# Kernel optimization log

Measured on AMD Instinct MI355X. Metric: run time of the kernel, lower is better.

## Reference

```python
import jax, jax.numpy as jnp
import numpy as np
from jax import lax

B, N, T, HOR, HID = 512, 128, 128, 32, 512


def _uni(k, shape, s):
    return jax.random.uniform(k, shape, jnp.float32, -s, s)


def setup_inputs() -> dict:
    key = jax.random.key(0)
    ks = jax.random.split(key, 24)
    s = 1.0 / np.sqrt(HID)
    inp = {"window": jax.random.normal(ks[0], (B * N, T), jnp.float32)}
    # encoder LSTM (2 layers, torch gate order i,f,g,o)
    inp["Wih0"] = _uni(ks[1], (4 * HID, N), s); inp["Whh0"] = _uni(ks[2], (4 * HID, HID), s)
    inp["bih0"] = _uni(ks[3], (4 * HID,), s);   inp["bhh0"] = _uni(ks[4], (4 * HID,), s)
    inp["Wih1"] = _uni(ks[5], (4 * HID, HID), s); inp["Whh1"] = _uni(ks[6], (4 * HID, HID), s)
    inp["bih1"] = _uni(ks[7], (4 * HID,), s);     inp["bhh1"] = _uni(ks[8], (4 * HID,), s)
    # decoder cells
    inp["Wc1i"] = _uni(ks[9], (4 * HID, N), s);   inp["Wc1h"] = _uni(ks[10], (4 * HID, HID), s)
    inp["bc1i"] = _uni(ks[11], (4 * HID,), s);    inp["bc1h"] = _uni(ks[12], (4 * HID,), s)
    inp["Wc2i"] = _uni(ks[13], (4 * HID, HID), s); inp["Wc2h"] = _uni(ks[14], (4 * HID, HID), s)
    inp["bc2i"] = _uni(ks[15], (4 * HID,), s);     inp["bc2h"] = _uni(ks[16], (4 * HID,), s)
    # output projection
    inp["Wp"] = _uni(ks[17], (N, HID), s); inp["bp"] = _uni(ks[18], (N,), s)
    # deterministic inverted-dropout masks
    keep_e = 0.75  # nn.LSTM inter-layer dropout p=0.25
    keep_d = 0.8   # F.dropout p=0.2 in decode loop
    inp["enc_mask"] = (jax.random.uniform(ks[19], (T, B, HID)) < keep_e).astype(jnp.float32) / keep_e
    inp["dec_h_mask"] = (jax.random.uniform(ks[20], (HOR - 1, B, HID)) < keep_d).astype(jnp.float32) / keep_d
    inp["dec_c_mask"] = (jax.random.uniform(ks[21], (HOR - 1, B, HID)) < keep_d).astype(jnp.float32) / keep_d
    return inp


def _cell(x, h, c, Wih, Whh, bih, bhh):
    g = x @ Wih.T + h @ Whh.T + (bih + bhh)
    i, f, gg, o = jnp.split(g, 4, axis=-1)
    c = jax.nn.sigmoid(f) * c + jax.nn.sigmoid(i) * jnp.tanh(gg)
    h = jax.nn.sigmoid(o) * jnp.tanh(c)
    return h, c


def _run_layer(xs, Wih, Whh, bih, bhh):
    # xs: [T, B, D] -> outputs [T, B, HID], final (h, c)
    h0 = jnp.zeros((xs.shape[1], HID), xs.dtype)
    def step(carry, x):
        h, c = carry
        h, c = _cell(x, h, c, Wih, Whh, bih, bhh)
        return (h, c), h
    (h, c), hs = lax.scan(step, (h0, h0), xs)
    return hs, h, c


def reference(window, Wih0, Whh0, bih0, bhh0, Wih1, Whh1, bih1, bhh1,
              Wc1i, Wc1h, bc1i, bc1h, Wc2i, Wc2h, bc2i, bc2h, Wp, bp,
              enc_mask, dec_h_mask, dec_c_mask):
    x = window.reshape(B, T, N).transpose(1, 0, 2)  # [T, B, N]
    hs0, h1, c1 = _run_layer(x, Wih0, Whh0, bih0, bhh0)
    hs0 = hs0 * enc_mask  # inter-layer dropout (training mode)
    _, h2, c2 = _run_layer(hs0, Wih1, Whh1, bih1, bhh1)

    def dec_step(carry, masks):
        h1, c1, h2, c2 = carry
        mh, mc = masks
        pred = h2 @ Wp.T + bp                       # [B, N]
        h1, c1 = _cell(pred, h1, c1, Wc1i, Wc1h, bc1i, bc1h)
        h1 = h1 * mh
        c1 = c1 * mc
        h2, c2 = _cell(h1, h2, c2, Wc2i, Wc2h, bc2i, bc2h)
        return (h1, c1, h2, c2), pred

    (h1, c1, h2, c2), preds = lax.scan(dec_step, (h1, c1, h2, c2), (dec_h_mask, dec_c_mask))
    final = h2 @ Wp.T + bp                          # [B, N]
    allp = jnp.concatenate([preds, final[None]], axis=0)  # [HOR, B, N]
    # torch: each pred.view(-1,1), cat dim=1 -> [B*N, HOR]
    return allp.transpose(1, 2, 0).reshape(B * N, HOR)
```

## Files before the change

kernel.cpp:

```cpp
#include <hip/hip_runtime.h>
#include <math.h>

#define HID 512
#define BAT 512
#define NIN 128
#define TST 128
#define HOR 32
#define SBZ ((size_t)BAT * HID)

using bf16x8 = __attribute__((ext_vector_type(8))) __bf16;
using f32x4  = __attribute__((ext_vector_type(4))) float;

__device__ __forceinline__ float sigf(float x) { return 1.0f / (1.0f + __expf(-x)); }
__device__ __forceinline__ float tanhfast(float x) { return 1.0f - 2.0f / (__expf(2.0f * x) + 1.0f); }

__device__ __forceinline__ short f2bf(float x) {
    union { float f; unsigned u; } v; v.f = x;
    unsigned r = (v.u + 0x7FFFu + ((v.u >> 16) & 1u)) >> 16;
    return (short)r;
}
__device__ __forceinline__ float bf2f(short s) {
    union { unsigned u; float f; } v; v.u = ((unsigned)(unsigned short)s) << 16;
    return v.f;
}
__device__ __forceinline__ bf16x8 asbf(f32x4 v) {
    union { f32x4 f; bf16x8 b; } u; u.f = v; return u.b;
}

__device__ __forceinline__ void gbar3(unsigned* bar, int bid, unsigned ep) {
    __syncthreads();
    if (threadIdx.x == 0) {
        unsigned* leaf = bar + ((unsigned)bid >> 3) * 32;
        unsigned* root = bar + 1024;
        unsigned* flag = bar + 1056;
        unsigned old = __hip_atomic_fetch_add(leaf, 1u, __ATOMIC_RELAXED, __HIP_MEMORY_SCOPE_AGENT);
        if (old == 8u * ep - 1u) {
            unsigned ro = __hip_atomic_fetch_add(root, 1u, __ATOMIC_RELAXED, __HIP_MEMORY_SCOPE_AGENT);
            if (ro == 32u * ep - 1u)
                __hip_atomic_store(flag, ep, __ATOMIC_RELAXED, __HIP_MEMORY_SCOPE_AGENT);
        }
        int spin = 0;
        while (__hip_atomic_load(flag, __ATOMIC_RELAXED, __HIP_MEMORY_SCOPE_AGENT) < ep) {
            __builtin_amdgcn_s_sleep(1);
            if (((++spin) & 63) == 0)
                __hip_atomic_fetch_add(flag, 0u, __ATOMIC_RELAXED, __HIP_MEMORY_SCOPE_AGENT);
        }
    }
    __syncthreads();
}


__global__ __launch_bounds__(256) void prep_w(const float* __restrict__ Wih,
                                              const float* __restrict__ Whh,
                                              short* __restrict__ W2, int Kx, int Kp) {
    size_t i = (size_t)blockIdx.x * 256 + threadIdx.x;
    if (i >= (size_t)2048 * Kp) return;
    int np = (int)(i / Kp), kp = (int)(i % Kp);
    int u = np >> 2, gate = np & 3;
    int on = gate * HID + u;
    float w = (kp < Kx) ? Wih[(size_t)on * Kx + kp] : Whh[(size_t)on * HID + (kp - Kx)];
    W2[i] = f2bf(w);
}

__global__ __launch_bounds__(256) void prep_x(const float* __restrict__ window,
                                              short* __restrict__ X2t) {
    size_t i = (size_t)blockIdx.x * 256 + threadIdx.x;
    if (i >= (size_t)TST * BAT * NIN) return;
    int n = (int)(i & 127);
    int b = (int)((i >> 7) & 511);
    int t = (int)(i >> 16);
    float x = window[(size_t)b * (TST * NIN) + (size_t)t * NIN + n];
    int rg = b >> 4;
    int l = (b & 15) + (((n >> 3) & 3) << 4);
    int e = n & 7;
    size_t base = (size_t)t * 65536 + ((size_t)(rg * 4 + (n >> 5)) << 9) + l * 8 + e;
    X2t[base] = f2bf(x);
}

__global__ __launch_bounds__(256) void prep_fuse(const float* __restrict__ Wc1i,
                                                 const float* __restrict__ Wp,
                                                 float* __restrict__ Wfuse) {
    size_t i = (size_t)blockIdx.x * 256 + threadIdx.x;
    if (i >= (size_t)2048 * 512) return;
    int on = (int)(i >> 9), k = (int)(i & 511);
    float s = 0.f;
    for (int n = 0; n < NIN; ++n) s += Wc1i[(size_t)on * NIN + n] * Wp[(size_t)n * HID + k];
    Wfuse[i] = s;
}

__global__ __launch_bounds__(256) void prep_badd(const float* __restrict__ Wc1i,
                                                 const float* __restrict__ bp,
                                                 float* __restrict__ badd) {
    int on = blockIdx.x * 256 + threadIdx.x;
    if (on >= 2048) return;
    float s = 0.f;
    for (int n = 0; n < NIN; ++n) s += Wc1i[(size_t)on * NIN + n] * bp[n];
    badd[on] = s;
}

__global__ __launch_bounds__(256) void prep_bias(const float* __restrict__ bih,
                                                 const float* __restrict__ bhh,
                                                 const float* __restrict__ badd,
                                                 float* __restrict__ bout) {
    int np = blockIdx.x * 256 + threadIdx.x;
    if (np >= 2048) return;
    int on = (np & 3) * HID + (np >> 2);
    float v = bih[on] + bhh[on];
    if (badd) v += badd[on];
    bout[np] = v;
}

__global__ __launch_bounds__(256) void prep_wp(const float* __restrict__ Wp,
                                               short* __restrict__ W2p) {
    int i = blockIdx.x * 256 + threadIdx.x;
    if (i >= 128 * 512) return;
    W2p[i] = f2bf(Wp[i]);
}


__device__ __forceinline__ void load_wres(char* lds, const short* Wg, int K) {
    const int tid = threadIdx.x;
    const int r = tid >> 4;
    const int cnt = K >> 7;
    const int jb = (tid & 15) * cnt;
    for (int q = 0; q < cnt; ++q) {
        int j = jb + q;
        bf16x8 v = *(const bf16x8*)(Wg + (size_t)r * K + j * 8);
        *(bf16x8*)(lds + j * 512 + r * 16) = v;
    }
}

__device__ __forceinline__ void pre_mask_asm(const float* msk, int mrow, int u0, float o[4]) {
    const int lane = threadIdx.x & 63;
    const float* p = msk + (size_t)(mrow + ((lane >> 3) << 2)) * HID + u0 + (lane & 7);
#pragma unroll
    for (int r = 0; r < 4; ++r)
        asm volatile("global_load_dword %0, %1, off" : "=v"(o[r]) : "v"(p + (size_t)r * HID));
}

template<int C0, int C1>
__device__ __forceinline__ void gemm_pipeC(
    const char* wres, const short* a0t, const short* a1t,
    int mb, f32x4 acc[2][2])
{
    constexpr int NKC = C0 + C1;
    constexpr int D = 16;
    const int lane = threadIdx.x & 63;
    const int arow = lane & 15, akg = lane >> 4;
    const size_t lb = (size_t)lane << 4;
    const char* base0 = (const char*)a0t;
    const char* base1 = (const char*)a1t;
    auto cptr = [&](int kc, int fh) -> const char* {
        return (kc < C0)
            ? base0 + (((size_t)(mb * 2 + fh) * C0 + kc) << 10) + lb
            : base1 + (((size_t)(mb * 2 + fh) * C1 + (kc - C0)) << 10) + lb;
    };
    f32x4 q0[D], q1[D];
#pragma unroll
    for (int i = 0; i < D; ++i) {
        asm volatile("global_load_dwordx4 %0, %1, off sc0 sc1" : "=v"(q0[i]) : "v"(cptr(i, 0)));
        asm volatile("global_load_dwordx4 %0, %1, off sc0 sc1" : "=v"(q1[i]) : "v"(cptr(i, 1)));
    }
#pragma unroll
    for (int kc = 0; kc < NKC; ++kc) {
        const int sl = kc % D;
        asm volatile("s_waitcnt vmcnt(%2)"
                     : "+v"(q0[sl]), "+v"(q1[sl])
                     : "i"((2 * ((NKC - kc) < D ? (NKC - kc) : D)) - 2));
        const bf16x8 fa0 = asbf(q0[sl]);
        const bf16x8 fa1 = asbf(q1[sl]);
        if (kc + D < NKC) {
            asm volatile("global_load_dwordx4 %0, %1, off sc0 sc1" : "=v"(q0[sl]) : "v"(cptr(kc + D, 0)));
            asm volatile("global_load_dwordx4 %0, %1, off sc0 sc1" : "=v"(q1[sl]) : "v"(cptr(kc + D, 1)));
        }
        const char* wrow = wres + (size_t)(((kc << 2) + akg) << 9);
        const bf16x8 fb0 = *(const bf16x8*)(wrow + (arow << 4));
        const bf16x8 fb1 = *(const bf16x8*)(wrow + ((16 + arow) << 4));
        acc[0][0] = __builtin_amdgcn_mfma_f32_16x16x32_bf16(fa0, fb0, acc[0][0], 0, 0, 0);
        acc[0][1] = __builtin_amdgcn_mfma_f32_16x16x32_bf16(fa0, fb1, acc[0][1], 0, 0, 0);
        acc[1][0] = __builtin_amdgcn_mfma_f32_16x16x32_bf16(fa1, fb0, acc[1][0], 0, 0, 0);
        acc[1][1] = __builtin_amdgcn_mfma_f32_16x16x32_bf16(fa1, fb1, acc[1][1], 0, 0, 0);
    }
    asm volatile("s_waitcnt vmcnt(0)");
}

__device__ __forceinline__ void cell_epi_r(
    char* scrw, f32x4 acc[2][2], float creg[4],
    int mb, int np0, const float* bias_p,
    const float* mh4, const float* mc4, const float* ma4,
    short* h2_out, short* h2_aux)
{
    const int lane = threadIdx.x & 63;
#pragma unroll
    for (int mi = 0; mi < 2; ++mi)
#pragma unroll
        for (int ni = 0; ni < 2; ++ni) {
            const int row = mi * 16 + ((lane >> 4) << 2);
            const int col = ni * 16 + (lane & 15);
#pragma unroll
            for (int r = 0; r < 4; ++r)
                *(float*)(scrw + (row + r) * 128 + (col << 2)) = acc[mi][ni][r];
        }
    asm volatile("s_waitcnt lgkmcnt(0)" ::: "memory");
    const int ul = lane & 7, g = lane >> 3;
    f32x4 gv[4];
#pragma unroll
    for (int r = 0; r < 4; ++r)
        gv[r] = *(const f32x4*)(scrw + ((g << 2) + r) * 128 + (ul << 4));
    asm volatile("s_waitcnt lgkmcnt(0)" ::: "memory");
    const float4 bs = *(const float4*)(bias_p + np0 + (ul << 2));
#pragma unroll
    for (int r = 0; r < 4; ++r) {
        const int m = (g << 2) + r;
        const int fh = m >> 4, r16 = m & 15;
        const float gi = gv[r][0] + bs.x, gf = gv[r][1] + bs.y;
        const float gg = gv[r][2] + bs.z, go = gv[r][3] + bs.w;
        const float cn = sigf(gf) * creg[r] + sigf(gi) * tanhfast(gg);
        const float h  = sigf(go) * tanhfast(cn);
        creg[r] = mc4 ? cn * mc4[r] : cn;
        const float hm = mh4 ? h * mh4[r] : h;
        const int idx2 = (r16 << 3) + ul;
        *(short*)(scrw + fh * 256 + idx2 * 2) = f2bf(hm);
        if (h2_aux)
            *(short*)(scrw + 512 + fh * 256 + idx2 * 2) = f2bf(h * ma4[r]);
    }
    const int u0l = np0 >> 2;
    const int c_hi = u0l >> 5, gsub = (u0l >> 3) & 3;
    unsigned vmain[2], vaux[2];
#pragma unroll
    for (int s = 0; s < 2; ++s)
        vmain[s] = *(const unsigned*)(scrw + s * 256 + (lane << 2));
    if (h2_aux)
#pragma unroll
        for (int s = 0; s < 2; ++s)
            vaux[s] = *(const unsigned*)(scrw + 512 + s * 256 + (lane << 2));
    asm volatile("s_waitcnt lgkmcnt(0)" ::: "memory");
#pragma unroll
    for (int s = 0; s < 2; ++s) {
        const unsigned* dst = (const unsigned*)(h2_out
            + ((size_t)((mb * 2 + s) * 16 + c_hi) << 9) + (gsub << 7)) + lane;
        asm volatile("global_store_dword %0, %1, off sc0 sc1" :: "v"(dst), "v"(vmain[s]));
    }
    if (h2_aux)
#pragma unroll
        for (int s = 0; s < 2; ++s) {
            const unsigned* dst = (const unsigned*)(h2_aux
                + ((size_t)((mb * 2 + s) * 16 + c_hi) << 9) + (gsub << 7)) + lane;
            asm volatile("global_store_dword %0, %1, off sc0 sc1" :: "v"(dst), "v"(vaux[s]));
        }
}


__global__ void __launch_bounds__(512, 2) persist_kernel(
    const short* X2t,
    const short* __restrict__ W0, const short* __restrict__ W1,
    const short* __restrict__ Wd1, const short* __restrict__ Wd2,
    short* hA0, short* hA1, short* hB0, short* hB1, short* hd0, short* hd1,
    short* hBall0, short* hBallR,
    const float* __restrict__ bias0, const float* __restrict__ bias1,
    const float* __restrict__ biasd1, const float* __restrict__ biasd2,
    const float* __restrict__ enc_mask, const float* __restrict__ dec_h_mask,
    const float* __restrict__ dec_c_mask, unsigned* bar)
{
    extern __shared__ __align__(16) char lds[];
    const int bid = blockIdx.x;
    const int xcd = bid & 7;
    const int half = xcd >> 2;
    const int m0 = ((xcd >> 1) & 1) * 256;
    const int np0 = (((bid >> 3) << 1) | (xcd & 1)) * 32;
    const int u0 = np0 >> 2;
    const int w = threadIdx.x >> 6;
    const int mb = (m0 >> 5) + w;
    const int mrow = m0 + (w << 5);
    char* scrw = lds + 65536 + (w << 12);
    float creg[4] = {0.f, 0.f, 0.f, 0.f};

    auto hball = [&](int s) -> short* {
        return (s == 0) ? hBall0 : hBallR + (size_t)(s - 1) * 262144;
    };

    load_wres(lds, (half ? W1 : W0) + (size_t)np0 * (half ? 1024 : 640), half ? 1024 : 640);
    __syncthreads();
    unsigned ep = 0;
    for (int tt = 0; tt <= TST; ++tt) {
        if (half == 0) {
            if (tt < TST) {
                const int t = tt;
                float ma[4];
                pre_mask_asm(enc_mask + (size_t)t * SBZ, mrow, u0, ma);
                f32x4 acc[2][2];
#pragma unroll
                for (int a = 0; a < 2; ++a)
#pragma unroll
                    for (int b2 = 0; b2 < 2; ++b2) acc[a][b2] = (f32x4){0.f, 0.f, 0.f, 0.f};
                gemm_pipeC<4, 16>(lds, X2t + (size_t)t * 65536, (t & 1) ? hA1 : hA0, mb, acc);
                cell_epi_r(scrw, acc, creg, mb, np0, bias0, nullptr, nullptr, ma,
                           (t & 1) ? hA0 : hA1, (t & 1) ? hd1 : hd0);
            }
        } else {
            if (tt >= 1) {
                const int t = tt - 1;
                f32x4 acc[2][2];
#pragma unroll
                for (int a = 0; a < 2; ++a)
#pragma unroll
                    for (int b2 = 0; b2 < 2; ++b2) acc[a][b2] = (f32x4){0.f, 0.f, 0.f, 0.f};
                gemm_pipeC<16, 16>(lds, (t & 1) ? hd1 : hd0, (t & 1) ? hB1 : hB0, mb, acc);
                short* outp = (t == TST - 1) ? hball(0) : ((t & 1) ? hB0 : hB1);
                cell_epi_r(scrw, acc, creg, mb, np0, bias1, nullptr, nullptr, nullptr,
                           outp, nullptr);
            }
        }
        gbar3(bar, bid, ++ep);
    }

    load_wres(lds, (half ? Wd2 : Wd1) + (size_t)np0 * 1024, 1024);
    __syncthreads();
    for (int s = 0; s < HOR - 1; ++s) {
        if (half == 0) {
            float mh[4], mc[4];
            pre_mask_asm(dec_h_mask + (size_t)s * SBZ, mrow, u0, mh);
            pre_mask_asm(dec_c_mask + (size_t)s * SBZ, mrow, u0, mc);
            f32x4 acc[2][2];
#pragma unroll
            for (int a = 0; a < 2; ++a)
#pragma unroll
                for (int b2 = 0; b2 < 2; ++b2) acc[a][b2] = (f32x4){0.f, 0.f, 0.f, 0.f};
            gemm_pipeC<16, 16>(lds, hball(s), (s & 1) ? hA1 : hA0, mb, acc);
            cell_epi_r(scrw, acc, creg, mb, np0, biasd1, mh, mc, nullptr,
                       (s & 1) ? hA0 : hA1, nullptr);
        }
        gbar3(bar, bid, ++ep);
        if (half == 1) {
            f32x4 acc[2][2];
#pragma unroll
            for (int a = 0; a < 2; ++a)
#pragma unroll
                for (int b2 = 0; b2 < 2; ++b2) acc[a][b2] = (f32x4){0.f, 0.f, 0.f, 0.f};
            gemm_pipeC<16, 16>(lds, (s & 1) ? hA0 : hA1, hball(s), mb, acc);
            cell_epi_r(scrw, acc, creg, mb, np0, biasd2, nullptr, nullptr, nullptr,
                       hball(s + 1), nullptr);
        }
        gbar3(bar, bid, ++ep);
    }
}


__global__ void __launch_bounds__(512, 2) proj_kernel(
    const short* hBall0, const short* hBallR, const short* __restrict__ W2p,
    const float* __restrict__ bp, float* __restrict__ pred_all)
{
    extern __shared__ __align__(16) char lds[];
    const int bid = blockIdx.x;
    const int s = bid >> 3, q = bid & 7;
    const int bh = q >> 2, n0p = (q & 3) * 32;
    load_wres(lds, W2p + (size_t)n0p * 512, 512);
    const int w = threadIdx.x >> 6, lane = threadIdx.x & 63;
    char* scrw = lds + 32768 + w * 4608;
    const int mb = bh * 8 + w;
    const short* A = (s == 0) ? hBall0 : hBallR + (size_t)(s - 1) * 262144;
    __syncthreads();
    f32x4 acc[2][2];
#pragma unroll
    for (int a = 0; a < 2; ++a)
#pragma unroll
        for (int b2 = 0; b2 < 2; ++b2) acc[a][b2] = (f32x4){0.f, 0.f, 0.f, 0.f};
    gemm_pipeC<16, 0>(lds, A, A, mb, acc);
#pragma unroll
    for (int mi = 0; mi < 2; ++mi)
#pragma unroll
        for (int ni = 0; ni < 2; ++ni) {
            const int row = mi * 16 + ((lane >> 4) << 2);
            const int col = ni * 16 + (lane & 15);
#pragma unroll
            for (int r = 0; r < 4; ++r)
                *(float*)(scrw + (row + r) * 144 + (col << 2)) = acc[mi][ni][r];
        }
    asm volatile("s_waitcnt lgkmcnt(0)" ::: "memory");
    const int rr = lane >> 1, hf = lane & 1;
    float* dst = pred_all + (size_t)s * (BAT * NIN)
               + (size_t)(bh * 256 + w * 32 + rr) * NIN + n0p + hf * 16;
#pragma unroll
    for (int t4 = 0; t4 < 4; ++t4) {
        f32x4 v = *(const f32x4*)(scrw + rr * 144 + hf * 64 + t4 * 16);
        const float4 b4 = *(const float4*)(bp + n0p + hf * 16 + t4 * 4);
        v[0] += b4.x; v[1] += b4.y; v[2] += b4.z; v[3] += b4.w;
        *(f32x4*)(dst + t4 * 4) = v;
    }
}

__global__ __launch_bounds__(256) void transpose_out(const float* __restrict__ pred_all,
                                                     float* __restrict__ out) {
    __shared__ float tl[32][65];
    const int base = blockIdx.x * 64;
    const int tid = threadIdx.x;
    for (int i = tid; i < 32 * 64; i += 256) {
        int s = i >> 6, f = i & 63;
        tl[s][f] = pred_all[(size_t)s * (BAT * NIN) + base + f];
    }
    __syncthreads();
    for (int i = tid; i < 64 * 32; i += 256) {
        int f = i >> 5, s = i & 31;
        out[(size_t)(base + f) * HOR + s] = tl[s][f];
    }
}


extern "C" void kernel_launch(void* const* d_in, const int* in_sizes, int n_in,
                              void* d_out, int out_size, void* d_ws, size_t ws_size,
                              hipStream_t stream) {
    (void)in_sizes; (void)n_in; (void)out_size; (void)ws_size;
    const float* window = (const float*)d_in[0];
    const float* Wih0 = (const float*)d_in[1];
    const float* Whh0 = (const float*)d_in[2];
    const float* bih0 = (const float*)d_in[3];
    const float* bhh0 = (const float*)d_in[4];
    const float* Wih1 = (const float*)d_in[5];
    const float* Whh1 = (const float*)d_in[6];
    const float* bih1 = (const float*)d_in[7];
    const float* bhh1 = (const float*)d_in[8];
    const float* Wc1i = (const float*)d_in[9];
    const float* Wc1h = (const float*)d_in[10];
    const float* bc1i = (const float*)d_in[11];
    const float* bc1h = (const float*)d_in[12];
    const float* Wc2i = (const float*)d_in[13];
    const float* Wc2h = (const float*)d_in[14];
    const float* bc2i = (const float*)d_in[15];
    const float* bc2h = (const float*)d_in[16];
    const float* Wp   = (const float*)d_in[17];
    const float* bp   = (const float*)d_in[18];
    const float* enc_mask   = (const float*)d_in[19];
    const float* dec_h_mask = (const float*)d_in[20];
    const float* dec_c_mask = (const float*)d_in[21];
    float* out = (float*)d_out;

    char* base = (char*)d_ws;
    size_t off = 0;
    auto take = [&](size_t bytes) -> char* {
        off = (off + 255) & ~(size_t)255;
        char* r = base + off; off += bytes; return r;
    };
    short* W2e0 = (short*)take((size_t)2048 * 640 * 2);
    short* W2e1 = (short*)take((size_t)2048 * 1024 * 2);
    short* W2d1 = (short*)take((size_t)2048 * 1024 * 2);
    short* W2d2 = (short*)take((size_t)2048 * 1024 * 2);
    short* W2p  = (short*)take((size_t)128 * 512 * 2);
    float* Wfuse = (float*)take((size_t)2048 * 512 * 4);
    float* badd  = (float*)take((size_t)2048 * 4);
    float* bias0 = (float*)take((size_t)2048 * 4);
    float* bias1 = (float*)take((size_t)2048 * 4);
    float* biasd1 = (float*)take((size_t)2048 * 4);
    float* biasd2 = (float*)take((size_t)2048 * 4);
    short* hA0 = (short*)take((size_t)262144 * 2);
    short* hA1 = (short*)take((size_t)262144 * 2);
    short* hB0 = (short*)take((size_t)262144 * 2);
    short* hB1 = (short*)take((size_t)262144 * 2);
    short* hd0 = (short*)take((size_t)262144 * 2);
    short* hd1 = (short*)take((size_t)262144 * 2);
    short* hBall0 = (short*)take((size_t)262144 * 2);
    float* pred_all = (float*)take((size_t)HOR * BAT * NIN * 4);
    unsigned* bars = (unsigned*)take(16384);
    short* X2t = (short*)take((size_t)TST * 65536 * 2);
    short* hBallR = X2t;

    prep_fuse<<<(2048 * 512 + 255) / 256, 256, 0, stream>>>(Wc1i, Wp, Wfuse);
    prep_badd<<<8, 256, 0, stream>>>(Wc1i, bp, badd);
    prep_wp<<<(128 * 512 + 255) / 256, 256, 0, stream>>>(Wp, W2p);
    prep_w<<<(2048 * 640 + 255) / 256, 256, 0, stream>>>(Wih0, Whh0, W2e0, NIN, 640);
    prep_w<<<(2048 * 1024 + 255) / 256, 256, 0, stream>>>(Wih1, Whh1, W2e1, HID, 1024);
    prep_w<<<(2048 * 1024 + 255) / 256, 256, 0, stream>>>(Wfuse, Wc1h, W2d1, HID, 1024);
    prep_w<<<(2048 * 1024 + 255) / 256, 256, 0, stream>>>(Wc2i, Wc2h, W2d2, HID, 1024);
    prep_bias<<<8, 256, 0, stream>>>(bih0, bhh0, nullptr, bias0);
    prep_bias<<<8, 256, 0, stream>>>(bih1, bhh1, nullptr, bias1);
    prep_bias<<<8, 256, 0, stream>>>(bc1i, bc1h, badd, biasd1);
    prep_bias<<<8, 256, 0, stream>>>(bc2i, bc2h, nullptr, biasd2);
    prep_x<<<(int)(((size_t)TST * BAT * NIN + 255) / 256), 256, 0, stream>>>(window, X2t);
    hipMemsetAsync(hA0, 0, (size_t)262144 * 2, stream);
    hipMemsetAsync(hB0, 0, (size_t)262144 * 2, stream);
    hipMemsetAsync(bars, 0, 16384, stream);

    hipFuncSetAttribute((const void*)persist_kernel, hipFuncAttributeMaxDynamicSharedMemorySize, 98304);
    hipFuncSetAttribute((const void*)proj_kernel, hipFuncAttributeMaxDynamicSharedMemorySize, 69632);

    persist_kernel<<<256, 512, 98304, stream>>>(
        X2t, W2e0, W2e1, W2d1, W2d2,
        hA0, hA1, hB0, hB1, hd0, hd1,
        hBall0, hBallR,
        bias0, bias1, biasd1, biasd2,
        enc_mask, dec_h_mask, dec_c_mask, bars);

    proj_kernel<<<256, 512, 69632, stream>>>(hBall0, hBallR, W2p, bp, pred_all);

    transpose_out<<<(BAT * NIN) / 64, 256, 0, stream>>>(pred_all, out);
}
```

Measured before the change: 1.763 ms.

## Widen persistent LSTM tiles to 64 columns on 128 blocks with fresh-buffer history

```diff
diff --git a/kernel.cpp b/kernel.cpp
--- a/kernel.cpp
+++ b/kernel.cpp
@@ -7,6 +7,8 @@
 #define TST 128
 #define HOR 32
 #define SBZ ((size_t)BAT * HID)
+#define SL 262144
+#define SLB 524288
 
 using bf16x8 = __attribute__((ext_vector_type(8))) __bf16;
 using f32x4  = __attribute__((ext_vector_type(4))) float;
@@ -27,7 +29,7 @@
     union { f32x4 f; bf16x8 b; } u; u.f = v; return u.b;
 }
 
-__device__ __forceinline__ void gbar3(unsigned* bar, int bid, unsigned ep) {
+__device__ __forceinline__ void gbar(unsigned* bar, int bid, unsigned ep) {
     __syncthreads();
     if (threadIdx.x == 0) {
         unsigned* leaf = bar + ((unsigned)bid >> 3) * 32;
@@ -36,7 +38,7 @@
         unsigned old = __hip_atomic_fetch_add(leaf, 1u, __ATOMIC_RELAXED, __HIP_MEMORY_SCOPE_AGENT);
         if (old == 8u * ep - 1u) {
             unsigned ro = __hip_atomic_fetch_add(root, 1u, __ATOMIC_RELAXED, __HIP_MEMORY_SCOPE_AGENT);
-            if (ro == 32u * ep - 1u)
+            if (ro == 16u * ep - 1u)
                 __hip_atomic_store(flag, ep, __ATOMIC_RELAXED, __HIP_MEMORY_SCOPE_AGENT);
         }
         int spin = 0;
@@ -118,7 +120,15 @@
 }
 
 
-__device__ __forceinline__ void load_wres(char* lds, const short* Wg, int K) {
+template<bool SC>
+__device__ __forceinline__ void gl16(f32x4& q, const char* p) {
+    if constexpr (SC)
+        asm volatile("global_load_dwordx4 %0, %1, off sc0 sc1" : "=v"(q) : "v"(p));
+    else
+        asm volatile("global_load_dwordx4 %0, %1, off" : "=v"(q) : "v"(p));
+}
+
+__device__ __forceinline__ void load_wres32(char* lds, const short* Wg, int K) {
     const int tid = threadIdx.x;
     const int r = tid >> 4;
     const int cnt = K >> 7;
@@ -130,6 +140,15 @@
     }
 }
 
+__device__ __forceinline__ void load_wres64(char* lds, const short* Wg, int K) {
+    const int r = threadIdx.x >> 3, jg = threadIdx.x & 7;
+    for (int q = 0; q < (K >> 6); ++q) {
+        int j = jg + (q << 3);
+        bf16x8 v = *(const bf16x8*)(Wg + (size_t)r * K + j * 8);
+        *(bf16x8*)(lds + (size_t)j * 1024 + r * 16) = v;
+    }
+}
+
 __device__ __forceinline__ void pre_mask_asm(const float* msk, int mrow, int u0, float o[4]) {
     const int lane = threadIdx.x & 63;
     const float* p = msk + (size_t)(mrow + ((lane >> 3) << 2)) * HID + u0 + (lane & 7);
@@ -138,8 +157,235 @@
         asm volatile("global_load_dword %0, %1, off" : "=v"(o[r]) : "v"(p + (size_t)r * HID));
 }
 
+template<int C0, int C1, bool SC>
+__device__ __forceinline__ void gemm64(
+    const char* wres, const short* a0t, const short* a1t,
+    int mb, f32x4 acc[2][4])
+{
+    constexpr int NKC = C0 + C1;
+    constexpr int D = 12;
+    const int lane = threadIdx.x & 63;
+    const int arow = lane & 15, akg = lane >> 4;
+    const size_t lb = (size_t)lane << 4;
+    const char* base0 = (const char*)a0t;
+    const char* base1 = (const char*)a1t;
+    auto cptr = [&](int kc, int fh) -> const char* {
+        return (kc < C0)
+            ? base0 + (((size_t)(mb * 2 + fh) * C0 + kc) << 10) + lb
+            : base1 + (((size_t)(mb * 2 + fh) * C1 + (kc - C0)) << 10) + lb;
+    };
+    f32x4 q0[D], q1[D];
+#pragma unroll
+    for (int i = 0; i < D; ++i) {
+        gl16<SC>(q0[i], cptr(i, 0));
+        gl16<SC>(q1[i], cptr(i, 1));
+    }
+#pragma unroll
+    for (int kc = 0; kc < NKC; ++kc) {
+        const int sl = kc % D;
+        asm volatile("s_waitcnt vmcnt(%2)"
+                     : "+v"(q0[sl]), "+v"(q1[sl])
+                     : "i"((2 * ((NKC - kc) < D ? (NKC - kc) : D)) - 2));
+        const bf16x8 fa0 = asbf(q0[sl]);
+        const bf16x8 fa1 = asbf(q1[sl]);
+        if (kc + D < NKC) {
+            gl16<SC>(q0[sl], cptr(kc + D, 0));
+            gl16<SC>(q1[sl], cptr(kc + D, 1));
+        }
+        const char* wrow = wres + (size_t)((kc << 2) + akg) * 1024;
+        bf16x8 fb[4];
+#pragma unroll
+        for (int nj = 0; nj < 4; ++nj)
+            fb[nj] = *(const bf16x8*)(wrow + ((nj * 16 + arow) << 4));
+#pragma unroll
+        for (int nj = 0; nj < 4; ++nj) {
+            acc[0][nj] = __builtin_amdgcn_mfma_f32_16x16x32_bf16(fa0, fb[nj], acc[0][nj], 0, 0, 0);
+            acc[1][nj] = __builtin_amdgcn_mfma_f32_16x16x32_bf16(fa1, fb[nj], acc[1][nj], 0, 0, 0);
+        }
+    }
+    asm volatile("s_waitcnt vmcnt(0)");
+}
+
+__device__ __forceinline__ void cell_epi64(
+    char* scrw, f32x4 acc[2][4], float creg[2][4], int mb, int np0,
+    const float* bias_p, const float* mh, const float* mc, const float* ma,
+    short* h_out, short* h_aux)
+{
+    const int lane = threadIdx.x & 63;
+#pragma unroll
+    for (int p = 0; p < 2; ++p) {
+        const int np0p = np0 + (p << 5);
+#pragma unroll
+        for (int mi = 0; mi < 2; ++mi)
+#pragma unroll
+            for (int nj = 0; nj < 2; ++nj) {
+                const int row = mi * 16 + ((lane >> 4) << 2);
+                const int col = nj * 16 + (lane & 15);
+#pragma unroll
+                for (int r = 0; r < 4; ++r)
+                    *(float*)(scrw + (row + r) * 128 + (col << 2)) = acc[mi][p * 2 + nj][r];
+            }
+        asm volatile("s_waitcnt lgkmcnt(0)" ::: "memory");
+        const int ul = lane & 7, g = lane >> 3;
+        f32x4 gv[4];
+#pragma unroll
+        for (int r = 0; r < 4; ++r)
+            gv[r] = *(const f32x4*)(scrw + ((g << 2) + r) * 128 + (ul << 4));
+        asm volatile("s_waitcnt lgkmcnt(0)" ::: "memory");
+        const float4 bs = *(const float4*)(bias_p + np0p + (ul << 2));
+#pragma unroll
+        for (int r = 0; r < 4; ++r) {
+            const int m = (g << 2) + r;
+            const int fh = m >> 4, r16 = m & 15;
+            const float gi = gv[r][0] + bs.x, gf = gv[r][1] + bs.y;
+            const float gg = gv[r][2] + bs.z, go = gv[r][3] + bs.w;
+            const float cn = sigf(gf) * creg[p][r] + sigf(gi) * tanhfast(gg);
+            const float h  = sigf(go) * tanhfast(cn);
+            creg[p][r] = mc ? cn * mc[p * 4 + r] : cn;
+            const float hm = mh ? h * mh[p * 4 + r] : h;
+            const int idx2 = (r16 << 3) + ul;
+            *(short*)(scrw + fh * 256 + idx2 * 2) = f2bf(hm);
+            if (h_aux)
+                *(short*)(scrw + 512 + fh * 256 + idx2 * 2) = f2bf(h * ma[p * 4 + r]);
+        }
+        const int u0p = np0p >> 2;
+        const int c_hi = u0p >> 5, gsub = (u0p >> 3) & 3;
+        unsigned vmain[2], vaux[2];
+#pragma unroll
+        for (int s = 0; s < 2; ++s)
+            vmain[s] = *(const unsigned*)(scrw + s * 256 + (lane << 2));
+        if (h_aux)
+#pragma unroll
+            for (int s = 0; s < 2; ++s)
+                vaux[s] = *(const unsigned*)(scrw + 512 + s * 256 + (lane << 2));
+        asm volatile("s_waitcnt lgkmcnt(0)" ::: "memory");
+#pragma unroll
+        for (int s = 0; s < 2; ++s) {
+            const unsigned* dst = (const unsigned*)(h_out
+                + ((size_t)((mb * 2 + s) * 16 + c_hi) << 9) + (gsub << 7)) + lane;
+            asm volatile("global_store_dword %0, %1, off sc0 sc1" :: "v"(dst), "v"(vmain[s]));
+        }
+        if (h_aux)
+#pragma unroll
+            for (int s = 0; s < 2; ++s) {
+                const unsigned* dst = (const unsigned*)(h_aux
+                    + ((size_t)((mb * 2 + s) * 16 + c_hi) << 9) + (gsub << 7)) + lane;
+                asm volatile("global_store_dword %0, %1, off sc0 sc1" :: "v"(dst), "v"(vaux[s]));
+            }
+    }
+}
+
+
+template<int FRESH>
+__global__ void __launch_bounds__(512, 1) persist_kernel(
+    const short* __restrict__ X2t,
+    const short* __restrict__ W0, const short* __restrict__ W1,
+    const short* __restrict__ Wd1, const short* __restrict__ Wd2,
+    short* hA, short* hd, short* hB,
+    short* hA1, short* hd1, short* hB1,
+    short* decA, short* hBall0, short* hBallR,
+    const float* __restrict__ bias0, const float* __restrict__ bias1,
+    const float* __restrict__ biasd1, const float* __restrict__ biasd2,
+    const float* __restrict__ enc_mask, const float* __restrict__ dec_h_mask,
+    const float* __restrict__ dec_c_mask, unsigned* bar)
+{
+    extern __shared__ __align__(16) char lds[];
+    const int bid = blockIdx.x;
+    const int xcd = bid & 7;
+    const int half = xcd >> 2;
+    const int m0 = ((xcd >> 1) & 1) * 256;
+    const int ntile = ((bid >> 3) << 1) | (xcd & 1);
+    const int np0 = ntile * 64;
+    const int u0 = np0 >> 2;
+    const int w = threadIdx.x >> 6;
+    const int mb = (m0 >> 5) + ((w >> 2) << 2) + (w & 3);
+    const int mrow = m0 + (w << 5);
+    char* scrw = lds + 131072 + (w << 12);
+    float creg[2][4] = {{0.f,0.f,0.f,0.f},{0.f,0.f,0.f,0.f}};
+
+    auto hA_rd = [&](int t) -> const short* { return FRESH ? hA + (size_t)t * SL : ((t & 1) ? hA1 : hA); };
+    auto hA_wr = [&](int t) -> short* { return FRESH ? hA + (size_t)(t + 1) * SL : ((t & 1) ? hA : hA1); };
+    auto hd_at = [&](int t) -> short* { return FRESH ? hd + (size_t)t * SL : ((t & 1) ? hd1 : hd); };
+    auto hB_rd = [&](int t) -> const short* { return FRESH ? hB + (size_t)t * SL : ((t & 1) ? hB1 : hB); };
+    auto hB_wr = [&](int t) -> short* { return FRESH ? hB + (size_t)(t + 1) * SL : ((t & 1) ? hB : hB1); };
+    auto decA_at = [&](int i) -> short* {
+        if (FRESH) return (i == 0) ? hA + (size_t)128 * SL : decA + (size_t)(i - 1) * SL;
+        return (i & 1) ? hA1 : hA;
+    };
+    auto hball = [&](int i) -> short* { return (i == 0) ? hBall0 : hBallR + (size_t)(i - 1) * SL; };
+
+    load_wres64(lds, (half ? W1 : W0) + (size_t)np0 * (half ? 1024 : 640), half ? 1024 : 640);
+    __syncthreads();
+    unsigned ep = 0;
+    for (int tt = 0; tt <= TST; ++tt) {
+        if (half == 0) {
+            if (tt < TST) {
+                const int t = tt;
+                float ma[8];
+                pre_mask_asm(enc_mask + (size_t)t * SBZ, mrow, u0, ma);
+                pre_mask_asm(enc_mask + (size_t)t * SBZ, mrow, u0 + 8, ma + 4);
+                f32x4 acc[2][4];
+#pragma unroll
+                for (int a = 0; a < 2; ++a)
+#pragma unroll
+                    for (int b2 = 0; b2 < 4; ++b2) acc[a][b2] = (f32x4){0.f, 0.f, 0.f, 0.f};
+                gemm64<4, 16, !FRESH>(lds, X2t + (size_t)t * 65536, hA_rd(t), mb, acc);
+                cell_epi64(scrw, acc, creg, mb, np0, bias0, nullptr, nullptr, ma,
+                           hA_wr(t), hd_at(t));
+            }
+        } else {
+            if (tt >= 1) {
+                const int t = tt - 1;
+                f32x4 acc[2][4];
+#pragma unroll
+                for (int a = 0; a < 2; ++a)
+#pragma unroll
+                    for (int b2 = 0; b2 < 4; ++b2) acc[a][b2] = (f32x4){0.f, 0.f, 0.f, 0.f};
+                gemm64<16, 16, !FRESH>(lds, hd_at(t), hB_rd(t), mb, acc);
+                short* outp = (t == TST - 1) ? hBall0 : hB_wr(t);
+                cell_epi64(scrw, acc, creg, mb, np0, bias1, nullptr, nullptr, nullptr,
+                           outp, nullptr);
+            }
+        }
+        gbar(bar, bid, ++ep);
+    }
+
+    load_wres64(lds, (half ? Wd2 : Wd1) + (size_t)np0 * 1024, 1024);
+    __syncthreads();
+    for (int s = 0; s < HOR - 1; ++s) {
+        if (half == 0) {
+            float mh[8], mc[8];
+            pre_mask_asm(dec_h_mask + (size_t)s * SBZ, mrow, u0, mh);
+            pre_mask_asm(dec_h_mask + (size_t)s * SBZ, mrow, u0 + 8, mh + 4);
+            pre_mask_asm(dec_c_mask + (size_t)s * SBZ, mrow, u0, mc);
+            pre_mask_asm(dec_c_mask + (size_t)s * SBZ, mrow, u0 + 8, mc + 4);
+            f32x4 acc[2][4];
+#pragma unroll
+            for (int a = 0; a < 2; ++a)
+#pragma unroll
+                for (int b2 = 0; b2 < 4; ++b2) acc[a][b2] = (f32x4){0.f, 0.f, 0.f, 0.f};
+            gemm64<16, 16, !FRESH>(lds, hball(s), decA_at(s), mb, acc);
+            cell_epi64(scrw, acc, creg, mb, np0, biasd1, mh, mc, nullptr,
+                       decA_at(s + 1), nullptr);
+        }
+        gbar(bar, bid, ++ep);
+        if (half == 1) {
+            f32x4 acc[2][4];
+#pragma unroll
+            for (int a = 0; a < 2; ++a)
+#pragma unroll
+                for (int b2 = 0; b2 < 4; ++b2) acc[a][b2] = (f32x4){0.f, 0.f, 0.f, 0.f};
+            gemm64<16, 16, !FRESH>(lds, decA_at(s + 1), hball(s), mb, acc);
+            cell_epi64(scrw, acc, creg, mb, np0, biasd2, nullptr, nullptr, nullptr,
+                       hball(s + 1), nullptr);
+        }
+        gbar(bar, bid, ++ep);
+    }
+}
+
+
 template<int C0, int C1>
-__device__ __forceinline__ void gemm_pipeC(
+__device__ __forceinline__ void gemm_pipeP(
     const char* wres, const short* a0t, const short* a1t,
     int mb, f32x4 acc[2][2])
 {
@@ -158,8 +404,8 @@
     f32x4 q0[D], q1[D];
 #pragma unroll
     for (int i = 0; i < D; ++i) {
-        asm volatile("global_load_dwordx4 %0, %1, off sc0 sc1" : "=v"(q0[i]) : "v"(cptr(i, 0)));
-        asm volatile("global_load_dwordx4 %0, %1, off sc0 sc1" : "=v"(q1[i]) : "v"(cptr(i, 1)));
+        gl16<true>(q0[i], cptr(i, 0));
+        gl16<true>(q1[i], cptr(i, 1));
     }
 #pragma unroll
     for (int kc = 0; kc < NKC; ++kc) {
@@ -170,8 +416,8 @@
         const bf16x8 fa0 = asbf(q0[sl]);
         const bf16x8 fa1 = asbf(q1[sl]);
         if (kc + D < NKC) {
-            asm volatile("global_load_dwordx4 %0, %1, off sc0 sc1" : "=v"(q0[sl]) : "v"(cptr(kc + D, 0)));
-            asm volatile("global_load_dwordx4 %0, %1, off sc0 sc1" : "=v"(q1[sl]) : "v"(cptr(kc + D, 1)));
+            gl16<true>(q0[sl], cptr(kc + D, 0));
+            gl16<true>(q1[sl], cptr(kc + D, 1));
         }
         const char* wrow = wres + (size_t)(((kc << 2) + akg) << 9);
         const bf16x8 fb0 = *(const bf16x8*)(wrow + (arow << 4));
@@ -183,168 +429,6 @@
     }
     asm volatile("s_waitcnt vmcnt(0)");
 }
-
-__device__ __forceinline__ void cell_epi_r(
-    char* scrw, f32x4 acc[2][2], float creg[4],
-    int mb, int np0, const float* bias_p,
-    const float* mh4, const float* mc4, const float* ma4,
-    short* h2_out, short* h2_aux)
-{
-    const int lane = threadIdx.x & 63;
-#pragma unroll
-    for (int mi = 0; mi < 2; ++mi)
-#pragma unroll
-        for (int ni = 0; ni < 2; ++ni) {
-            const int row = mi * 16 + ((lane >> 4) << 2);
-            const int col = ni * 16 + (lane & 15);
-#pragma unroll
-            for (int r = 0; r < 4; ++r)
-                *(float*)(scrw + (row + r) * 128 + (col << 2)) = acc[mi][ni][r];
-        }
-    asm volatile("s_waitcnt lgkmcnt(0)" ::: "memory");
-    const int ul = lane & 7, g = lane >> 3;
-    f32x4 gv[4];
-#pragma unroll
-    for (int r = 0; r < 4; ++r)
-        gv[r] = *(const f32x4*)(scrw + ((g << 2) + r) * 128 + (ul << 4));
-    asm volatile("s_waitcnt lgkmcnt(0)" ::: "memory");
-    const float4 bs = *(const float4*)(bias_p + np0 + (ul << 2));
-#pragma unroll
-    for (int r = 0; r < 4; ++r) {
-        const int m = (g << 2) + r;
-        const int fh = m >> 4, r16 = m & 15;
-        const float gi = gv[r][0] + bs.x, gf = gv[r][1] + bs.y;
-        const float gg = gv[r][2] + bs.z, go = gv[r][3] + bs.w;
-        const float cn = sigf(gf) * creg[r] + sigf(gi) * tanhfast(gg);
-        const float h  = sigf(go) * tanhfast(cn);
-        creg[r] = mc4 ? cn * mc4[r] : cn;
-        const float hm = mh4 ? h * mh4[r] : h;
-        const int idx2 = (r16 << 3) + ul;
-        *(short*)(scrw + fh * 256 + idx2 * 2) = f2bf(hm);
-        if (h2_aux)
-            *(short*)(scrw + 512 + fh * 256 + idx2 * 2) = f2bf(h * ma4[r]);
-    }
-    const int u0l = np0 >> 2;
-    const int c_hi = u0l >> 5, gsub = (u0l >> 3) & 3;
-    unsigned vmain[2], vaux[2];
-#pragma unroll
-    for (int s = 0; s < 2; ++s)
-        vmain[s] = *(const unsigned*)(scrw + s * 256 + (lane << 2));
-    if (h2_aux)
-#pragma unroll
-        for (int s = 0; s < 2; ++s)
-            vaux[s] = *(const unsigned*)(scrw + 512 + s * 256 + (lane << 2));
-    asm volatile("s_waitcnt lgkmcnt(0)" ::: "memory");
-#pragma unroll
-    for (int s = 0; s < 2; ++s) {
-        const unsigned* dst = (const unsigned*)(h2_out
-            + ((size_t)((mb * 2 + s) * 16 + c_hi) << 9) + (gsub << 7)) + lane;
-        asm volatile("global_store_dword %0, %1, off sc0 sc1" :: "v"(dst), "v"(vmain[s]));
-    }
-    if (h2_aux)
-#pragma unroll
-        for (int s = 0; s < 2; ++s) {
-            const unsigned* dst = (const unsigned*)(h2_aux
-                + ((size_t)((mb * 2 + s) * 16 + c_hi) << 9) + (gsub << 7)) + lane;
-            asm volatile("global_store_dword %0, %1, off sc0 sc1" :: "v"(dst), "v"(vaux[s]));
-        }
-}
-
-
-__global__ void __launch_bounds__(512, 2) persist_kernel(
-    const short* X2t,
-    const short* __restrict__ W0, const short* __restrict__ W1,
-    const short* __restrict__ Wd1, const short* __restrict__ Wd2,
-    short* hA0, short* hA1, short* hB0, short* hB1, short* hd0, short* hd1,
-    short* hBall0, short* hBallR,
-    const float* __restrict__ bias0, const float* __restrict__ bias1,
-    const float* __restrict__ biasd1, const float* __restrict__ biasd2,
-    const float* __restrict__ enc_mask, const float* __restrict__ dec_h_mask,
-    const float* __restrict__ dec_c_mask, unsigned* bar)
-{
-    extern __shared__ __align__(16) char lds[];
-    const int bid = blockIdx.x;
-    const int xcd = bid & 7;
-    const int half = xcd >> 2;
-    const int m0 = ((xcd >> 1) & 1) * 256;
-    const int np0 = (((bid >> 3) << 1) | (xcd & 1)) * 32;
-    const int u0 = np0 >> 2;
-    const int w = threadIdx.x >> 6;
-    const int mb = (m0 >> 5) + w;
-    const int mrow = m0 + (w << 5);
-    char* scrw = lds + 65536 + (w << 12);
-    float creg[4] = {0.f, 0.f, 0.f, 0.f};
-
-    auto hball = [&](int s) -> short* {
-        return (s == 0) ? hBall0 : hBallR + (size_t)(s - 1) * 262144;
-    };
-
-    load_wres(lds, (half ? W1 : W0) + (size_t)np0 * (half ? 1024 : 640), half ? 1024 : 640);
-    __syncthreads();
-    unsigned ep = 0;
-    for (int tt = 0; tt <= TST; ++tt) {
-        if (half == 0) {
-            if (tt < TST) {
-                const int t = tt;
-                float ma[4];
-                pre_mask_asm(enc_mask + (size_t)t * SBZ, mrow, u0, ma);
-                f32x4 acc[2][2];
-#pragma unroll
-                for (int a = 0; a < 2; ++a)
-#pragma unroll
-                    for (int b2 = 0; b2 < 2; ++b2) acc[a][b2] = (f32x4){0.f, 0.f, 0.f, 0.f};
-                gemm_pipeC<4, 16>(lds, X2t + (size_t)t * 65536, (t & 1) ? hA1 : hA0, mb, acc);
-                cell_epi_r(scrw, acc, creg, mb, np0, bias0, nullptr, nullptr, ma,
-                           (t & 1) ? hA0 : hA1, (t & 1) ? hd1 : hd0);
-            }
-        } else {
-            if (tt >= 1) {
-                const int t = tt - 1;
-                f32x4 acc[2][2];
-#pragma unroll
-                for (int a = 0; a < 2; ++a)
-#pragma unroll
-                    for (int b2 = 0; b2 < 2; ++b2) acc[a][b2] = (f32x4){0.f, 0.f, 0.f, 0.f};
-                gemm_pipeC<16, 16>(lds, (t & 1) ? hd1 : hd0, (t & 1) ? hB1 : hB0, mb, acc);
-                short* outp = (t == TST - 1) ? hball(0) : ((t & 1) ? hB0 : hB1);
-                cell_epi_r(scrw, acc, creg, mb, np0, bias1, nullptr, nullptr, nullptr,
-                           outp, nullptr);
-            }
-        }
-        gbar3(bar, bid, ++ep);
-    }
-
-    load_wres(lds, (half ? Wd2 : Wd1) + (size_t)np0 * 1024, 1024);
-    __syncthreads();
-    for (int s = 0; s < HOR - 1; ++s) {
-        if (half == 0) {
-            float mh[4], mc[4];
-            pre_mask_asm(dec_h_mask + (size_t)s * SBZ, mrow, u0, mh);
-            pre_mask_asm(dec_c_mask + (size_t)s * SBZ, mrow, u0, mc);
-            f32x4 acc[2][2];
-#pragma unroll
-            for (int a = 0; a < 2; ++a)
-#pragma unroll
-                for (int b2 = 0; b2 < 2; ++b2) acc[a][b2] = (f32x4){0.f, 0.f, 0.f, 0.f};
-            gemm_pipeC<16, 16>(lds, hball(s), (s & 1) ? hA1 : hA0, mb, acc);
-            cell_epi_r(scrw, acc, creg, mb, np0, biasd1, mh, mc, nullptr,
-                       (s & 1) ? hA0 : hA1, nullptr);
-        }
-        gbar3(bar, bid, ++ep);
-        if (half == 1) {
-            f32x4 acc[2][2];
-#pragma unroll
-            for (int a = 0; a < 2; ++a)
-#pragma unroll
-                for (int b2 = 0; b2 < 2; ++b2) acc[a][b2] = (f32x4){0.f, 0.f, 0.f, 0.f};
-            gemm_pipeC<16, 16>(lds, (s & 1) ? hA0 : hA1, hball(s), mb, acc);
-            cell_epi_r(scrw, acc, creg, mb, np0, biasd2, nullptr, nullptr, nullptr,
-                       hball(s + 1), nullptr);
-        }
-        gbar3(bar, bid, ++ep);
-    }
-}
-
 
 __global__ void __launch_bounds__(512, 2) proj_kernel(
     const short* hBall0, const short* hBallR, const short* __restrict__ W2p,
@@ -354,18 +438,18 @@
     const int bid = blockIdx.x;
     const int s = bid >> 3, q = bid & 7;
     const int bh = q >> 2, n0p = (q & 3) * 32;
-    load_wres(lds, W2p + (size_t)n0p * 512, 512);
+    load_wres32(lds, W2p + (size_t)n0p * 512, 512);
     const int w = threadIdx.x >> 6, lane = threadIdx.x & 63;
     char* scrw = lds + 32768 + w * 4608;
     const int mb = bh * 8 + w;
-    const short* A = (s == 0) ? hBall0 : hBallR + (size_t)(s - 1) * 262144;
+    const short* A = (s == 0) ? hBall0 : hBallR + (size_t)(s - 1) * SL;
     __syncthreads();
     f32x4 acc[2][2];
 #pragma unroll
     for (int a = 0; a < 2; ++a)
 #pragma unroll
         for (int b2 = 0; b2 < 2; ++b2) acc[a][b2] = (f32x4){0.f, 0.f, 0.f, 0.f};
-    gemm_pipeC<16, 0>(lds, A, A, mb, acc);
+    gemm_pipeP<16, 0>(lds, A, A, mb, acc);
 #pragma unroll
     for (int mi = 0; mi < 2; ++mi)
 #pragma unroll
@@ -409,7 +493,7 @@
 extern "C" void kernel_launch(void* const* d_in, const int* in_sizes, int n_in,
                               void* d_out, int out_size, void* d_ws, size_t ws_size,
                               hipStream_t stream) {
-    (void)in_sizes; (void)n_in; (void)out_size; (void)ws_size;
+    (void)in_sizes; (void)n_in; (void)out_size;
     const float* window = (const float*)d_in[0];
     const float* Wih0 = (const float*)d_in[1];
     const float* Whh0 = (const float*)d_in[2];
@@ -451,17 +535,27 @@
     float* bias1 = (float*)take((size_t)2048 * 4);
     float* biasd1 = (float*)take((size_t)2048 * 4);
     float* biasd2 = (float*)take((size_t)2048 * 4);
-    short* hA0 = (short*)take((size_t)262144 * 2);
-    short* hA1 = (short*)take((size_t)262144 * 2);
-    short* hB0 = (short*)take((size_t)262144 * 2);
-    short* hB1 = (short*)take((size_t)262144 * 2);
-    short* hd0 = (short*)take((size_t)262144 * 2);
-    short* hd1 = (short*)take((size_t)262144 * 2);
-    short* hBall0 = (short*)take((size_t)262144 * 2);
+    short* hBall0 = (short*)take(SLB);
     float* pred_all = (float*)take((size_t)HOR * BAT * NIN * 4);
     unsigned* bars = (unsigned*)take(16384);
     short* X2t = (short*)take((size_t)TST * 65536 * 2);
-    short* hBallR = X2t;
+
+    const size_t fresh_need = (size_t)448 * SLB + 65536;
+    bool FRESHM = (ws_size >= off + fresh_need);
+    short *hAp, *hdp, *hBp, *hA1p = nullptr, *hd1p = nullptr, *hB1p = nullptr;
+    short *decAp = nullptr, *hballRp;
+    if (FRESHM) {
+        hAp    = (short*)take((size_t)129 * SLB);
+        hdp    = (short*)take((size_t)128 * SLB);
+        hBp    = (short*)take((size_t)129 * SLB);
+        decAp  = (short*)take((size_t)31 * SLB);
+        hballRp = (short*)take((size_t)31 * SLB);
+    } else {
+        hAp  = (short*)take(SLB); hA1p = (short*)take(SLB);
+        hdp  = (short*)take(SLB); hd1p = (short*)take(SLB);
+        hBp  = (short*)take(SLB); hB1p = (short*)take(SLB);
+        hballRp = X2t;
+    }
 
     prep_fuse<<<(2048 * 512 + 255) / 256, 256, 0, stream>>>(Wc1i, Wp, Wfuse);
     prep_badd<<<8, 256, 0, stream>>>(Wc1i, bp, badd);
@@ -475,21 +569,33 @@
     prep_bias<<<8, 256, 0, stream>>>(bc1i, bc1h, badd, biasd1);
     prep_bias<<<8, 256, 0, stream>>>(bc2i, bc2h, nullptr, biasd2);
     prep_x<<<(int)(((size_t)TST * BAT * NIN + 255) / 256), 256, 0, stream>>>(window, X2t);
-    hipMemsetAsync(hA0, 0, (size_t)262144 * 2, stream);
-    hipMemsetAsync(hB0, 0, (size_t)262144 * 2, stream);
+    hipMemsetAsync(hAp, 0, SLB, stream);
+    hipMemsetAsync(hBp, 0, SLB, stream);
     hipMemsetAsync(bars, 0, 16384, stream);
 
-    hipFuncSetAttribute((const void*)persist_kernel, hipFuncAttributeMaxDynamicSharedMemorySize, 98304);
-    hipFuncSetAttribute((const void*)proj_kernel, hipFuncAttributeMaxDynamicSharedMemorySize, 69632);
-
-    persist_kernel<<<256, 512, 98304, stream>>>(
-        X2t, W2e0, W2e1, W2d1, W2d2,
-        hA0, hA1, hB0, hB1, hd0, hd1,
-        hBall0, hBallR,
-        bias0, bias1, biasd1, biasd2,
-        enc_mask, dec_h_mask, dec_c_mask, bars);
-
-    proj_kernel<<<256, 512, 69632, stream>>>(hBall0, hBallR, W2p, bp, pred_all);
+    if (FRESHM) {
+        hipFuncSetAttribute((const void*)&persist_kernel<1>,
+                            hipFuncAttributeMaxDynamicSharedMemorySize, 163840);
+        persist_kernel<1><<<128, 512, 163840, stream>>>(
+            X2t, W2e0, W2e1, W2d1, W2d2,
+            hAp, hdp, hBp, hA1p, hd1p, hB1p,
+            decAp, hBall0, hballRp,
+            bias0, bias1, biasd1, biasd2,
+            enc_mask, dec_h_mask, dec_c_mask, bars);
+    } else {
+        hipFuncSetAttribute((const void*)&persist_kernel<0>,
+                            hipFuncAttributeMaxDynamicSharedMemorySize, 163840);
+        persist_kernel<0><<<128, 512, 163840, stream>>>(
+            X2t, W2e0, W2e1, W2d1, W2d2,
+            hAp, hdp, hBp, hA1p, hd1p, hB1p,
+            decAp, hBall0, hballRp,
+            bias0, bias1, biasd1, biasd2,
+            enc_mask, dec_h_mask, dec_c_mask, bars);
+    }
+
+    hipFuncSetAttribute((const void*)&proj_kernel,
+                        hipFuncAttributeMaxDynamicSharedMemorySize, 69632);
+    proj_kernel<<<256, 512, 69632, stream>>>(hBall0, hballRp, W2p, bp, pred_all);
 
     transpose_out<<<(BAT * NIN) / 64, 256, 0, stream>>>(pred_all, out);
 }
```

New measurement: 2.292 ms. 30.0% more time.
